# Kernel optimization log

Measured on AMD Instinct MI355X. Metric: run time of the kernel, lower is better.

The kernel has to match this reference:

```python
import jax, jax.numpy as jnp
import numpy as np

N_NODES = 50000
N_EDGES = 800000
N_GRAPHS = 128
IN_DIM = 256
OUT_DIM = 128
N_LAYERS = 3
NEG_SLOPE = 0.01  # nn.LeakyReLU default


def setup_inputs() -> dict:
    key = jax.random.key(0)
    ks = jax.random.split(key, 10)
    feat = jax.random.normal(ks[0], (N_NODES, IN_DIM), jnp.float32)
    src = jax.random.randint(ks[1], (N_EDGES,), 0, N_NODES, jnp.int32)
    dst = jax.random.randint(ks[2], (N_EDGES,), 0, N_NODES, jnp.int32)
    graph_ids = jnp.sort(jax.random.randint(ks[3], (N_NODES,), 0, N_GRAPHS, jnp.int32))
    s_in = 1.0 / np.sqrt(IN_DIM).astype(np.float32)
    s_out = 1.0 / np.sqrt(OUT_DIM).astype(np.float32)
    w_red = jax.random.uniform(ks[4], (IN_DIM, OUT_DIM), jnp.float32, -s_in, s_in)
    b_red = jax.random.uniform(ks[5], (OUT_DIM,), jnp.float32, -s_in, s_in)
    w_gcn = jax.random.uniform(ks[6], (N_LAYERS, OUT_DIM, OUT_DIM), jnp.float32, -s_out, s_out)
    b_gcn = jnp.zeros((N_LAYERS, OUT_DIM), jnp.float32)  # DGL GraphConv bias init = zeros
    w_cls = jax.random.uniform(ks[7], (OUT_DIM, 2), jnp.float32, -s_out, s_out)
    b_cls = jax.random.uniform(ks[8], (2,), jnp.float32, -s_out, s_out)
    return dict(feat=feat, src=src, dst=dst, graph_ids=graph_ids,
                w_red=w_red, b_red=b_red, w_gcn=w_gcn, b_gcn=b_gcn,
                w_cls=w_cls, b_cls=b_cls)


def _graph_conv(x, src, dst, w, b, out_norm, in_norm):
    # DGL GraphConv, norm='both': h = D_in^{-1/2} A D_out^{-1/2} x W + b
    xs = x * out_norm[:, None]                                   # [N, d] source normalization
    agg = jax.ops.segment_sum(xs[src], dst, num_segments=x.shape[0])  # gather -> scatter-add
    return (agg * in_norm[:, None]) @ w + b


def reference(feat, src, dst, graph_ids, w_red, b_red, w_gcn, b_gcn, w_cls, b_cls):
    n = feat.shape[0]
    ones = jnp.ones((src.shape[0],), feat.dtype)
    out_deg = jax.ops.segment_sum(ones, src, num_segments=n)
    in_deg = jax.ops.segment_sum(ones, dst, num_segments=n)
    out_norm = jnp.maximum(out_deg, 1.0) ** -0.5  # DGL clamps degree to >=1
    in_norm = jnp.maximum(in_deg, 1.0) ** -0.5
    h0 = feat @ w_red + b_red  # Dropout(0.2) in eval mode = identity
    # Faithful to source: every layer consumes h0 (node_features never updated);
    # only the last layer's activation survives the loop.
    out = h0
    for i in range(N_LAYERS):
        out = jax.nn.leaky_relu(
            _graph_conv(h0, src, dst, w_gcn[i], b_gcn[i], out_norm, in_norm), NEG_SLOPE)
    g = jax.ops.segment_sum(out, graph_ids, num_segments=N_GRAPHS)  # sum readout per graph
    return g @ w_cls + b_cls  # [N_GRAPHS, 2]
```

## Files before the change

### kernel.cpp

```cpp
#include <hip/hip_runtime.h>

#define N_NODES 50000
#define N_EDGES 800000
#define N_GRAPHS 128
#define IN_DIM 256
#define OUT_DIM 128
#define NEG_SLOPE 0.01f

#define RCHUNK 64
#define NB_SCAN ((N_NODES + 255) / 256)

#define NSLICE 4
#define SLICE 12544
#define NTOT (NSLICE * SLICE)
#define NCHUNK 64
#define NE4 (N_EDGES / 4)
#define QPC (NE4 / NCHUNK)

typedef __attribute__((ext_vector_type(8))) short bf16x8;
typedef __attribute__((ext_vector_type(4))) float f32x4;
typedef unsigned short ushort_t;
typedef unsigned int uint_t;

__device__ inline ushort_t f2b(float f) {
    union { float f; unsigned u; } c{f};
    unsigned r = c.u + 0x7FFFu + ((c.u >> 16) & 1u);
    return (ushort_t)(r >> 16);
}
__device__ inline float b2f(ushort_t u) {
    union { unsigned u; float f; } c{(unsigned)u << 16};
    return c.f;
}
__device__ inline float blo(uint_t v) {
    union { unsigned u; float f; } c{v << 16};
    return c.f;
}
__device__ inline float bhi(uint_t v) {
    union { unsigned u; float f; } c{v & 0xFFFF0000u};
    return c.f;
}

__global__ __launch_bounds__(256) void deg_kernel(const int4* __restrict__ src4,
                                                  const int4* __restrict__ dst4,
                                                  int* __restrict__ rep) {
    __shared__ int bins[SLICE];
    int b     = blockIdx.x;
    int hist  = b >> 8;
    int rem   = b & 255;
    int slice = rem >> 6;
    int chunk = rem & 63;
    const int4* ea = hist ? dst4 : src4;
    int lo = slice * SLICE;

    for (int i = threadIdx.x; i < SLICE; i += 256) bins[i] = 0;
    __syncthreads();

    int q0 = chunk * QPC;
    int q1 = q0 + QPC;
    for (int q = q0 + threadIdx.x; q < q1; q += 256) {
        int4 e = ea[q];
        unsigned a0 = (unsigned)(e.x - lo); if (a0 < SLICE) atomicAdd(&bins[a0], 1);
        unsigned a1 = (unsigned)(e.y - lo); if (a1 < SLICE) atomicAdd(&bins[a1], 1);
        unsigned a2 = (unsigned)(e.z - lo); if (a2 < SLICE) atomicAdd(&bins[a2], 1);
        unsigned a3 = (unsigned)(e.w - lo); if (a3 < SLICE) atomicAdd(&bins[a3], 1);
    }
    __syncthreads();

    int* rp = rep + (size_t)(hist * NCHUNK + chunk) * NTOT + lo;
    for (int i = threadIdx.x; i < SLICE / 4; i += 256)
        *(int4*)&rp[i * 4] = *(const int4*)&bins[i * 4];
}

__global__ __launch_bounds__(256) void norm_kernel(int* __restrict__ rep,
                                                   float* __restrict__ out_norm,
                                                   float* __restrict__ in_norm,
                                                   int* __restrict__ deg_in_tot) {
    int i = blockIdx.x * 256 + threadIdx.x;
    if (i < N_NODES) {
        int so = 0;
#pragma unroll
        for (int c = 0; c < NCHUNK; ++c) so += rep[(size_t)c * NTOT + i];
        int si = 0;
#pragma unroll
        for (int c = 0; c < NCHUNK; ++c) {
            size_t off = (size_t)(NCHUNK + c) * NTOT + i;
            int v = rep[off];
            rep[off] = si;
            si += v;
        }
        deg_in_tot[i] = si;
        int dq = so > 1 ? so : 1;
        int di = si > 1 ? si : 1;
        out_norm[i] = rsqrtf((float)dq);
        in_norm[i]  = rsqrtf((float)di);
    }
}

__global__ __launch_bounds__(256) void partial_kernel(const int* __restrict__ deg_in,
                                                      int* __restrict__ bsum) {
    __shared__ int red[256];
    int t   = threadIdx.x;
    int idx = blockIdx.x * 256 + t;
    red[t] = (idx < N_NODES) ? deg_in[idx] : 0;
    __syncthreads();
    for (int off = 128; off > 0; off >>= 1) {
        if (t < off) red[t] += red[t + off];
        __syncthreads();
    }
    if (t == 0) bsum[blockIdx.x] = red[0];
}

__global__ __launch_bounds__(256) void scan_bsums(const int* __restrict__ bsum,
                                                  int* __restrict__ bofs,
                                                  int* __restrict__ row_ofs) {
    __shared__ int sh[256];
    int t = threadIdx.x;
    int v = (t < NB_SCAN) ? bsum[t] : 0;
    sh[t] = v;
    __syncthreads();
    for (int off = 1; off < 256; off <<= 1) {
        int a = sh[t];
        int b = (t >= off) ? sh[t - off] : 0;
        __syncthreads();
        sh[t] = a + b;
        __syncthreads();
    }
    if (t < NB_SCAN) bofs[t] = sh[t] - v;
    if (t == 255)    row_ofs[N_NODES] = sh[NB_SCAN - 1];
}

__global__ __launch_bounds__(256) void fill_kernel(const int* __restrict__ deg_in,
                                                   const int* __restrict__ bofs,
                                                   int* __restrict__ row_ofs) {
    __shared__ int sh[256];
    int t   = threadIdx.x;
    int idx = blockIdx.x * 256 + t;
    int v   = (idx < N_NODES) ? deg_in[idx] : 0;
    sh[t] = v;
    __syncthreads();
    for (int off = 1; off < 256; off <<= 1) {
        int a = sh[t];
        int b = (t >= off) ? sh[t - off] : 0;
        __syncthreads();
        sh[t] = a + b;
        __syncthreads();
    }
    if (idx < N_NODES) row_ofs[idx] = bofs[blockIdx.x] + sh[t] - v;
}

__global__ __launch_bounds__(256) void build_kernel(const int4* __restrict__ src4,
                                                    const int4* __restrict__ dst4,
                                                    const int* __restrict__ row_ofs,
                                                    const int* __restrict__ rep,
                                                    int* __restrict__ esrc) {
    __shared__ int cur[SLICE];
    int b     = blockIdx.x;
    int slice = b >> 6;
    int chunk = b & 63;
    int lo    = slice * SLICE;
    const int* rel = rep + (size_t)(NCHUNK + chunk) * NTOT + lo;

    for (int i = threadIdx.x; i < SLICE; i += 256) {
        int n = lo + i;
        int r = (n < N_NODES) ? row_ofs[n] : 0;
        cur[i] = r + rel[i];
    }
    __syncthreads();

    int q0 = chunk * QPC;
    int q1 = q0 + QPC;
    for (int q = q0 + threadIdx.x; q < q1; q += 256) {
        int4 s = src4[q];
        int4 d = dst4[q];
        unsigned a0 = (unsigned)(d.x - lo); if (a0 < SLICE) esrc[atomicAdd(&cur[a0], 1)] = s.x;
        unsigned a1 = (unsigned)(d.y - lo); if (a1 < SLICE) esrc[atomicAdd(&cur[a1], 1)] = s.y;
        unsigned a2 = (unsigned)(d.z - lo); if (a2 < SLICE) esrc[atomicAdd(&cur[a2], 1)] = s.z;
        unsigned a3 = (unsigned)(d.w - lo); if (a3 < SLICE) esrc[atomicAdd(&cur[a3], 1)] = s.w;
    }
}

__global__ __launch_bounds__(128) void wc_kernel(const float* __restrict__ w_red,
                                                 const float* __restrict__ b_red,
                                                 const float* __restrict__ w2,
                                                 ushort_t* __restrict__ Wcs,
                                                 float* __restrict__ bc) {
    int j = threadIdx.x;
    int i = blockIdx.x;
    const float* vin = (i < IN_DIM) ? (w_red + (size_t)i * OUT_DIM) : b_red;
    float s = 0.f;
    for (int k = 0; k < OUT_DIM; ++k) s = fmaf(vin[k], w2[k * OUT_DIM + j], s);
    if (i < IN_DIM) Wcs[(size_t)j * IN_DIM + i] = f2b(s);
    else            bc[j] = s;
}

__global__ __launch_bounds__(256) void gemm_z(const float* __restrict__ feat,
                                              const ushort_t* __restrict__ Wcs,
                                              const float* __restrict__ bc,
                                              const float* __restrict__ out_norm,
                                              ushort_t* __restrict__ zb) {
    __shared__ ushort_t Bs[64 * IN_DIM];
    int t    = threadIdx.x;
    int lane = t & 63;
    int wv   = t >> 6;
    int bm   = blockIdx.x * 64 + wv * 16;
    int bn0  = blockIdx.y * 64;
    int mrow = lane & 15;
    int kg   = lane >> 4;
    int gm   = bm + mrow;

    {
        const char* wsrc = (const char*)(Wcs + (size_t)bn0 * IN_DIM);
        char* bdst = (char*)Bs;
#pragma unroll
        for (int p = 0; p < 8; ++p) {
            int d  = p * 4096 + t * 16;
            int ds = d ^ (((d >> 9) & 7) << 4);
            *(int4*)(bdst + ds) = *(const int4*)(wsrc + d);
        }
    }
    __syncthreads();

    f32x4 acc[4];
#pragma unroll
    for (int nt = 0; nt < 4; ++nt) acc[nt] = (f32x4){0.f, 0.f, 0.f, 0.f};

    int boff[4];
#pragma unroll
    for (int nt = 0; nt < 4; ++nt) {
        int n = nt * 16 + mrow;
        boff[nt] = n * 512 + ((kg * 16) ^ ((n & 7) << 4));
    }
    const char* bsp = (const char*)Bs;

    bool valid = gm < N_NODES;
    const float* fp = feat + (size_t)(valid ? gm : 0) * IN_DIM + kg * 8;
    const float4 zf4 = make_float4(0.f, 0.f, 0.f, 0.f);

    float4 a0c = valid ? *(const float4*)(fp + 0) : zf4;
    float4 a1c = valid ? *(const float4*)(fp + 4) : zf4;
    float4 a0n = zf4, a1n = zf4;

#pragma unroll
    for (int kt = 0; kt < IN_DIM / 32; ++kt) {
        if (kt < IN_DIM / 32 - 1) {
            a0n = valid ? *(const float4*)(fp + (kt + 1) * 32) : zf4;
            a1n = valid ? *(const float4*)(fp + (kt + 1) * 32 + 4) : zf4;
        }
        bf16x8 af;
        af[0] = (short)f2b(a0c.x); af[1] = (short)f2b(a0c.y);
        af[2] = (short)f2b(a0c.z); af[3] = (short)f2b(a0c.w);
        af[4] = (short)f2b(a1c.x); af[5] = (short)f2b(a1c.y);
        af[6] = (short)f2b(a1c.z); af[7] = (short)f2b(a1c.w);
#pragma unroll
        for (int nt = 0; nt < 4; ++nt) {
            bf16x8 bf = *(const bf16x8*)(bsp + (boff[nt] ^ (kt << 6)));
            acc[nt] = __builtin_amdgcn_mfma_f32_16x16x32_bf16(af, bf, acc[nt], 0, 0, 0);
        }
        a0c = a0n; a1c = a1n;
    }

    float on[4];
#pragma unroll
    for (int r = 0; r < 4; ++r) {
        int row = bm + kg * 4 + r;
        on[r] = (row < N_NODES) ? out_norm[row] : 0.f;
    }
#pragma unroll
    for (int nt = 0; nt < 4; ++nt) {
        int col = bn0 + nt * 16 + mrow;
        float bcv = bc[col];
#pragma unroll
        for (int r = 0; r < 4; ++r) {
            int row = bm + kg * 4 + r;
            if (row < N_NODES)
                zb[(size_t)row * OUT_DIM + col] = f2b(on[r] * (acc[nt][r] + bcv));
        }
    }
}

__global__ __launch_bounds__(256) void gather_kernel(const uint_t* __restrict__ zb2,
                                                     const int* __restrict__ esrc,
                                                     const int* __restrict__ row_ofs,
                                                     const float* __restrict__ in_norm,
                                                     const float* __restrict__ b2,
                                                     uint_t* __restrict__ hb2) {
    int n    = blockIdx.x * 4 + (threadIdx.x >> 6);
    int lane = threadIdx.x & 63;
    if (n >= N_NODES) return;
    int e0 = row_ofs[n];
    int e1 = row_ofs[n + 1];
    float acc0 = 0.f, acc1 = 0.f;
    int e = e0;
    for (; e + 4 <= e1; e += 4) {
        int sa = esrc[e + 0];
        int sb = esrc[e + 1];
        int sc = esrc[e + 2];
        int sd = esrc[e + 3];
        uint_t va = zb2[(size_t)sa * 64 + lane];
        uint_t vb = zb2[(size_t)sb * 64 + lane];
        uint_t vc = zb2[(size_t)sc * 64 + lane];
        uint_t vd = zb2[(size_t)sd * 64 + lane];
        acc0 += (blo(va) + blo(vb)) + (blo(vc) + blo(vd));
        acc1 += (bhi(va) + bhi(vb)) + (bhi(vc) + bhi(vd));
    }
    for (; e < e1; ++e) {
        uint_t v = zb2[(size_t)esrc[e] * 64 + lane];
        acc0 += blo(v);
        acc1 += bhi(v);
    }
    float inn = in_norm[n];
    float2 bj = *(const float2*)&b2[2 * lane];
    float h0 = fmaf(inn, acc0, bj.x);
    float h1 = fmaf(inn, acc1, bj.y);
    h0 = (h0 > 0.f) ? h0 : NEG_SLOPE * h0;
    h1 = (h1 > 0.f) ? h1 : NEG_SLOPE * h1;
    hb2[(size_t)n * 64 + lane] = (uint_t)f2b(h0) | ((uint_t)f2b(h1) << 16);
}

__global__ __launch_bounds__(128) void readout_kernel(const ushort_t* __restrict__ hb,
                                                      const int* __restrict__ gids,
                                                      float* __restrict__ g) {
    int j    = threadIdx.x;
    int n0   = blockIdx.x * RCHUNK;
    int nend = n0 + RCHUNK;
    if (nend > N_NODES) nend = N_NODES;
    float acc = 0.f;
    int   cur = gids[n0];
    for (int n = n0; n < nend; ++n) {
        int gid = gids[n];
        if (gid != cur) {
            atomicAdd(&g[cur * OUT_DIM + j], acc);
            acc = 0.f;
            cur = gid;
        }
        acc += b2f(hb[(size_t)n * OUT_DIM + j]);
    }
    atomicAdd(&g[cur * OUT_DIM + j], acc);
}

__global__ __launch_bounds__(256) void cls_kernel(const float* __restrict__ g,
                                                  const float* __restrict__ w_cls,
                                                  const float* __restrict__ b_cls,
                                                  float* __restrict__ out) {
    int t  = threadIdx.x;
    int gr = t >> 1;
    int c  = t & 1;
    float s = b_cls[c];
    for (int k = 0; k < OUT_DIM; ++k) s = fmaf(g[gr * OUT_DIM + k], w_cls[k * 2 + c], s);
    out[t] = s;
}

extern "C" void kernel_launch(void* const* d_in, const int* in_sizes, int n_in,
                              void* d_out, int out_size, void* d_ws, size_t ws_size,
                              hipStream_t stream) {
    const float* feat  = (const float*)d_in[0];
    const int*   src   = (const int*)d_in[1];
    const int*   dst   = (const int*)d_in[2];
    const int*   gids  = (const int*)d_in[3];
    const float* w_red = (const float*)d_in[4];
    const float* b_red = (const float*)d_in[5];
    const float* w_gcn = (const float*)d_in[6];
    const float* b_gcn = (const float*)d_in[7];
    const float* w_cls = (const float*)d_in[8];
    const float* b_cls = (const float*)d_in[9];
    float* out = (float*)d_out;

    float* z        = (float*)d_ws;
    float* h        = z + (size_t)N_NODES * OUT_DIM;
    float* out_norm = h + (size_t)N_NODES * OUT_DIM;
    float* in_norm  = out_norm + N_NODES;
    int*   deg_in   = (int*)(in_norm + N_NODES);
    int*   row_ofs  = deg_in + N_NODES;
    int*   esrc     = row_ofs + N_NODES + 1;
    int*   bsum     = esrc + N_EDGES;
    int*   bofs     = bsum + NB_SCAN;
    ushort_t* Wcs   = (ushort_t*)(bofs + NB_SCAN);
    float* bc       = (float*)(Wcs + IN_DIM * OUT_DIM);
    float* g        = bc + OUT_DIM;

    ushort_t* zb = (ushort_t*)z;
    ushort_t* hb = (ushort_t*)h;

    int* rep = (int*)z;

    const float* w2 = w_gcn + 2 * OUT_DIM * OUT_DIM;
    const float* b2 = b_gcn + 2 * OUT_DIM;

    hipMemsetAsync(g, 0, (size_t)N_GRAPHS * OUT_DIM * sizeof(float), stream);

    deg_kernel<<<2 * NSLICE * NCHUNK, 256, 0, stream>>>((const int4*)src, (const int4*)dst, rep);
    norm_kernel<<<(N_NODES + 255) / 256, 256, 0, stream>>>(rep, out_norm, in_norm, deg_in);
    partial_kernel<<<NB_SCAN, 256, 0, stream>>>(deg_in, bsum);
    scan_bsums<<<1, 256, 0, stream>>>(bsum, bofs, row_ofs);
    fill_kernel<<<NB_SCAN, 256, 0, stream>>>(deg_in, bofs, row_ofs);
    build_kernel<<<NSLICE * NCHUNK, 256, 0, stream>>>((const int4*)src, (const int4*)dst,
                                                      row_ofs, rep, esrc);
    wc_kernel<<<IN_DIM + 1, OUT_DIM, 0, stream>>>(w_red, b_red, w2, Wcs, bc);
    gemm_z<<<dim3((N_NODES + 63) / 64, 2), 256, 0, stream>>>(feat, Wcs, bc, out_norm, zb);
    gather_kernel<<<(N_NODES + 3) / 4, 256, 0, stream>>>((const uint_t*)zb, esrc, row_ofs,
                                                         in_norm, b2, (uint_t*)hb);
    readout_kernel<<<(N_NODES + RCHUNK - 1) / RCHUNK, 128, 0, stream>>>(hb, gids, g);
    cls_kernel<<<1, 256, 0, stream>>>(g, w_cls, b_cls, out);
}
```

Baseline: 175.8 us.

## Column-partition node features for cache-resident gather; shrink degree histograms to 16-bit

Stores the z and h feature matrices column-partitioned into four 32-feature slabs (64 bytes per node), and launches the gather over each slab separately. Each partition (~3.2 MB) is meant to stay in cache during the random neighbor gathers. Within a wavefront, four edge streams of 16 lanes are reduced with shuffles. The per-chunk degree histograms are stored as 16-bit values to halve that traffic, and the block partial-sum kernel is fused into norm_kernel. The gather launches four times more blocks, only 16 of 64 lanes store, and the unrolled multi-edge loads are removed.

```diff
diff --git a/kernel.cpp b/kernel.cpp
--- a/kernel.cpp
+++ b/kernel.cpp
@@ -16,6 +16,7 @@
 #define NCHUNK 64
 #define NE4 (N_EDGES / 4)
 #define QPC (NE4 / NCHUNK)
+#define NPB 12500
 
 typedef __attribute__((ext_vector_type(8))) short bf16x8;
 typedef __attribute__((ext_vector_type(4))) float f32x4;
@@ -42,7 +43,7 @@
 
 __global__ __launch_bounds__(256) void deg_kernel(const int4* __restrict__ src4,
                                                   const int4* __restrict__ dst4,
-                                                  int* __restrict__ rep) {
+                                                  ushort_t* __restrict__ rep) {
     __shared__ int bins[SLICE];
     int b     = blockIdx.x;
     int hist  = b >> 8;
@@ -66,16 +67,20 @@
     }
     __syncthreads();
 
-    int* rp = rep + (size_t)(hist * NCHUNK + chunk) * NTOT + lo;
-    for (int i = threadIdx.x; i < SLICE / 4; i += 256)
-        *(int4*)&rp[i * 4] = *(const int4*)&bins[i * 4];
-}
-
-__global__ __launch_bounds__(256) void norm_kernel(int* __restrict__ rep,
+    uint_t* rp32 = (uint_t*)(rep + (size_t)(hist * NCHUNK + chunk) * NTOT + lo);
+    for (int i = threadIdx.x; i < SLICE / 2; i += 256)
+        rp32[i] = (uint_t)(bins[2 * i] | (bins[2 * i + 1] << 16));
+}
+
+__global__ __launch_bounds__(256) void norm_kernel(ushort_t* __restrict__ rep,
                                                    float* __restrict__ out_norm,
                                                    float* __restrict__ in_norm,
-                                                   int* __restrict__ deg_in_tot) {
-    int i = blockIdx.x * 256 + threadIdx.x;
+                                                   int* __restrict__ deg_in_tot,
+                                                   int* __restrict__ bsum) {
+    __shared__ int red[256];
+    int t = threadIdx.x;
+    int i = blockIdx.x * 256 + t;
+    int si_keep = 0;
     if (i < N_NODES) {
         int so = 0;
 #pragma unroll
@@ -85,23 +90,17 @@
         for (int c = 0; c < NCHUNK; ++c) {
             size_t off = (size_t)(NCHUNK + c) * NTOT + i;
             int v = rep[off];
-            rep[off] = si;
+            rep[off] = (ushort_t)si;
             si += v;
         }
         deg_in_tot[i] = si;
+        si_keep = si;
         int dq = so > 1 ? so : 1;
         int di = si > 1 ? si : 1;
         out_norm[i] = rsqrtf((float)dq);
         in_norm[i]  = rsqrtf((float)di);
     }
-}
-
-__global__ __launch_bounds__(256) void partial_kernel(const int* __restrict__ deg_in,
-                                                      int* __restrict__ bsum) {
-    __shared__ int red[256];
-    int t   = threadIdx.x;
-    int idx = blockIdx.x * 256 + t;
-    red[t] = (idx < N_NODES) ? deg_in[idx] : 0;
+    red[t] = si_keep;
     __syncthreads();
     for (int off = 128; off > 0; off >>= 1) {
         if (t < off) red[t] += red[t + off];
@@ -151,19 +150,19 @@
 __global__ __launch_bounds__(256) void build_kernel(const int4* __restrict__ src4,
                                                     const int4* __restrict__ dst4,
                                                     const int* __restrict__ row_ofs,
-                                                    const int* __restrict__ rep,
+                                                    const ushort_t* __restrict__ rep,
                                                     int* __restrict__ esrc) {
     __shared__ int cur[SLICE];
     int b     = blockIdx.x;
     int slice = b >> 6;
     int chunk = b & 63;
     int lo    = slice * SLICE;
-    const int* rel = rep + (size_t)(NCHUNK + chunk) * NTOT + lo;
+    const ushort_t* rel = rep + (size_t)(NCHUNK + chunk) * NTOT + lo;
 
     for (int i = threadIdx.x; i < SLICE; i += 256) {
         int n = lo + i;
         int r = (n < N_NODES) ? row_ofs[n] : 0;
-        cur[i] = r + rel[i];
+        cur[i] = r + (int)rel[i];
     }
     __syncthreads();
 
@@ -197,7 +196,7 @@
                                               const ushort_t* __restrict__ Wcs,
                                               const float* __restrict__ bc,
                                               const float* __restrict__ out_norm,
-                                              ushort_t* __restrict__ zb) {
+                                              ushort_t* __restrict__ zt) {
     __shared__ ushort_t Bs[64 * IN_DIM];
     int t    = threadIdx.x;
     int lane = t & 63;
@@ -269,58 +268,57 @@
     for (int nt = 0; nt < 4; ++nt) {
         int col = bn0 + nt * 16 + mrow;
         float bcv = bc[col];
+        size_t base = ((size_t)(col >> 5) * N_NODES) * 32 + (col & 31);
 #pragma unroll
         for (int r = 0; r < 4; ++r) {
             int row = bm + kg * 4 + r;
             if (row < N_NODES)
-                zb[(size_t)row * OUT_DIM + col] = f2b(on[r] * (acc[nt][r] + bcv));
-        }
-    }
-}
-
-__global__ __launch_bounds__(256) void gather_kernel(const uint_t* __restrict__ zb2,
+                zt[base + (size_t)row * 32] = f2b(on[r] * (acc[nt][r] + bcv));
+        }
+    }
+}
+
+__global__ __launch_bounds__(256) void gather_kernel(const uint_t* __restrict__ zt,
                                                      const int* __restrict__ esrc,
                                                      const int* __restrict__ row_ofs,
                                                      const float* __restrict__ in_norm,
                                                      const float* __restrict__ b2,
-                                                     uint_t* __restrict__ hb2) {
-    int n    = blockIdx.x * 4 + (threadIdx.x >> 6);
+                                                     uint_t* __restrict__ ht) {
+    int gb   = blockIdx.x;
+    int p    = gb / NPB;
+    int n    = (gb % NPB) * 4 + (threadIdx.x >> 6);
     int lane = threadIdx.x & 63;
-    if (n >= N_NODES) return;
+    int es   = lane >> 4;
+    int cp   = lane & 15;
     int e0 = row_ofs[n];
     int e1 = row_ofs[n + 1];
+    const uint_t* zp = zt + (size_t)p * N_NODES * 16;
     float acc0 = 0.f, acc1 = 0.f;
-    int e = e0;
-    for (; e + 4 <= e1; e += 4) {
-        int sa = esrc[e + 0];
-        int sb = esrc[e + 1];
-        int sc = esrc[e + 2];
-        int sd = esrc[e + 3];
-        uint_t va = zb2[(size_t)sa * 64 + lane];
-        uint_t vb = zb2[(size_t)sb * 64 + lane];
-        uint_t vc = zb2[(size_t)sc * 64 + lane];
-        uint_t vd = zb2[(size_t)sd * 64 + lane];
-        acc0 += (blo(va) + blo(vb)) + (blo(vc) + blo(vd));
-        acc1 += (bhi(va) + bhi(vb)) + (bhi(vc) + bhi(vd));
-    }
-    for (; e < e1; ++e) {
-        uint_t v = zb2[(size_t)esrc[e] * 64 + lane];
+    for (int e = e0 + es; e < e1; e += 4) {
+        int s = esrc[e];
+        uint_t v = zp[(size_t)s * 16 + cp];
         acc0 += blo(v);
         acc1 += bhi(v);
     }
+    acc0 += __shfl_xor(acc0, 16, 64);
+    acc1 += __shfl_xor(acc1, 16, 64);
+    acc0 += __shfl_xor(acc0, 32, 64);
+    acc1 += __shfl_xor(acc1, 32, 64);
     float inn = in_norm[n];
-    float2 bj = *(const float2*)&b2[2 * lane];
+    float2 bj = *(const float2*)&b2[p * 32 + cp * 2];
     float h0 = fmaf(inn, acc0, bj.x);
     float h1 = fmaf(inn, acc1, bj.y);
     h0 = (h0 > 0.f) ? h0 : NEG_SLOPE * h0;
     h1 = (h1 > 0.f) ? h1 : NEG_SLOPE * h1;
-    hb2[(size_t)n * 64 + lane] = (uint_t)f2b(h0) | ((uint_t)f2b(h1) << 16);
-}
-
-__global__ __launch_bounds__(128) void readout_kernel(const ushort_t* __restrict__ hb,
+    if (lane < 16)
+        ht[((size_t)p * N_NODES + n) * 16 + cp] = (uint_t)f2b(h0) | ((uint_t)f2b(h1) << 16);
+}
+
+__global__ __launch_bounds__(128) void readout_kernel(const ushort_t* __restrict__ ht,
                                                       const int* __restrict__ gids,
                                                       float* __restrict__ g) {
     int j    = threadIdx.x;
+    size_t cbase = ((size_t)(j >> 5) * N_NODES) * 32 + (j & 31);
     int n0   = blockIdx.x * RCHUNK;
     int nend = n0 + RCHUNK;
     if (nend > N_NODES) nend = N_NODES;
@@ -333,7 +331,7 @@
             acc = 0.f;
             cur = gid;
         }
-        acc += b2f(hb[(size_t)n * OUT_DIM + j]);
+        acc += b2f(ht[cbase + (size_t)n * 32]);
     }
     atomicAdd(&g[cur * OUT_DIM + j], acc);
 }
@@ -378,10 +376,10 @@
     float* bc       = (float*)(Wcs + IN_DIM * OUT_DIM);
     float* g        = bc + OUT_DIM;
 
-    ushort_t* zb = (ushort_t*)z;
-    ushort_t* hb = (ushort_t*)h;
-
-    int* rep = (int*)z;
+    ushort_t* zt = (ushort_t*)z;
+    ushort_t* ht = (ushort_t*)h;
+
+    ushort_t* rep = (ushort_t*)z;
 
     const float* w2 = w_gcn + 2 * OUT_DIM * OUT_DIM;
     const float* b2 = b_gcn + 2 * OUT_DIM;
@@ -389,16 +387,15 @@
     hipMemsetAsync(g, 0, (size_t)N_GRAPHS * OUT_DIM * sizeof(float), stream);
 
     deg_kernel<<<2 * NSLICE * NCHUNK, 256, 0, stream>>>((const int4*)src, (const int4*)dst, rep);
-    norm_kernel<<<(N_NODES + 255) / 256, 256, 0, stream>>>(rep, out_norm, in_norm, deg_in);
-    partial_kernel<<<NB_SCAN, 256, 0, stream>>>(deg_in, bsum);
+    norm_kernel<<<NB_SCAN, 256, 0, stream>>>(rep, out_norm, in_norm, deg_in, bsum);
     scan_bsums<<<1, 256, 0, stream>>>(bsum, bofs, row_ofs);
     fill_kernel<<<NB_SCAN, 256, 0, stream>>>(deg_in, bofs, row_ofs);
     build_kernel<<<NSLICE * NCHUNK, 256, 0, stream>>>((const int4*)src, (const int4*)dst,
                                                       row_ofs, rep, esrc);
     wc_kernel<<<IN_DIM + 1, OUT_DIM, 0, stream>>>(w_red, b_red, w2, Wcs, bc);
-    gemm_z<<<dim3((N_NODES + 63) / 64, 2), 256, 0, stream>>>(feat, Wcs, bc, out_norm, zb);
-    gather_kernel<<<(N_NODES + 3) / 4, 256, 0, stream>>>((const uint_t*)zb, esrc, row_ofs,
-                                                         in_norm, b2, (uint_t*)hb);
-    readout_kernel<<<(N_NODES + RCHUNK - 1) / RCHUNK, 128, 0, stream>>>(hb, gids, g);
+    gemm_z<<<dim3((N_NODES + 63) / 64, 2), 256, 0, stream>>>(feat, Wcs, bc, out_norm, zt);
+    gather_kernel<<<4 * NPB, 256, 0, stream>>>((const uint_t*)zt, esrc, row_ofs,
+                                               in_norm, b2, (uint_t*)ht);
+    readout_kernel<<<(N_NODES + RCHUNK - 1) / RCHUNK, 128, 0, stream>>>(ht, gids, g);
     cls_kernel<<<1, 256, 0, stream>>>(g, w_cls, b_cls, out);
 }
```

New measurement: 227.0 us. 1.29x slower.
